# Kernel tuning notes

Hardware: AMD Instinct MI355X
Metric: run time of the kernel (lower is better)

The kernel has to match this reference:

```python
import jax, jax.numpy as jnp
import numpy as np

B, N, H = 32, 64, 128
RBF_DIM, GH, SCATTER, OUT = 32, 256, 64, 256
CUTOFF, PMAX = 6.0, 256
MAXZ, ZEMB, EDIM, NE, PH = 100, 32, 32, 64, 256


def _lin(k, din, dout):
    k1, k2 = jax.random.split(k)
    s = 1.0 / np.sqrt(din)
    W = jax.random.uniform(k1, (din, dout), minval=-s, maxval=s)
    b = jax.random.uniform(k2, (dout,), minval=-s, maxval=s)
    return W, b


def setup_inputs() -> dict:
    key = jax.random.key(0)
    ks = jax.random.split(key, 16)
    h = jax.random.normal(ks[0], (B, N, H), dtype=jnp.float32)
    z = jax.random.randint(ks[1], (B, N), 1, MAXZ + 1)
    pos = jax.random.normal(ks[2], (B, N, 3), dtype=jnp.float32) * 2.0
    mask = jax.random.randint(ks[3], (B, N), 0, 2).astype(bool).at[:, 0].set(True)
    e_feat = jax.random.normal(ks[4], (NE, EDIM), dtype=jnp.float32)
    z_emb = jax.random.normal(ks[5], (MAXZ + 1, ZEMB), dtype=jnp.float32)
    gm_W1, gm_b1 = _lin(ks[6], 2 * H + 3 * RBF_DIM + 1, GH)
    gm_W2, gm_b2 = _lin(ks[7], GH, GH)
    gm_W3, gm_b3 = _lin(ks[8], GH, SCATTER)
    pe_W1, pe_b1 = _lin(ks[9], 2 * ZEMB + EDIM, PH)
    pe_W2, pe_b2 = _lin(ks[10], PH, PH)
    pe_W3, pe_b3 = _lin(ks[11], PH, SCATTER)
    op_W1, op_b1 = _lin(ks[12], SCATTER, GH)
    op_W2, op_b2 = _lin(ks[13], GH, OUT)
    return dict(h=h, z=z, pos=pos, mask=mask, e_feat=e_feat, z_emb=z_emb,
                gm_W1=gm_W1, gm_b1=gm_b1, gm_W2=gm_W2, gm_b2=gm_b2, gm_W3=gm_W3, gm_b3=gm_b3,
                pe_W1=pe_W1, pe_b1=pe_b1, pe_W2=pe_W2, pe_b2=pe_b2, pe_W3=pe_W3, pe_b3=pe_b3,
                op_W1=op_W1, op_b1=op_b1, op_W2=op_W2, op_b2=op_b2, absorber_index=0)


def _mlp3(x, W1, b1, W2, b2, W3, b3):
    x = jax.nn.silu(x @ W1 + b1)
    x = jax.nn.silu(x @ W2 + b2)
    return x @ W3 + b3


def _rbf(x):
    centers = jnp.linspace(0.0, CUTOFF, RBF_DIM)
    delta = CUTOFF / (RBF_DIM - 1)
    gamma = 1.0 / (delta * delta + 1e-12)
    return jnp.exp(-gamma * (x[..., None] - centers) ** 2)


def _norm(v):
    # numerically safe euclidean norm over last axis
    return jnp.sqrt(jnp.sum(v * v, axis=-1) + 1e-12)


def _forward(h, z, pos, mask, e_feat, z_emb,
             gm_W1, gm_b1, gm_W2, gm_b2, gm_W3, gm_b3,
             pe_W1, pe_b1, pe_W2, pe_b2, pe_W3, pe_b3,
             op_W1, op_b1, op_W2, op_b2, absorber_index):
    pos0 = pos[:, absorber_index][:, None, :]                       # [B,1,3]
    r = _norm(pos - pos0)                                           # [B,N]
    valid = mask & (jnp.arange(N)[None, :] != absorber_index) & (r <= CUTOFF)
    # enumerate pairs (j<k) in lexicographic order == torch.combinations of sorted where()
    ju, ku = jnp.triu_indices(N, k=1)                               # [Np]
    pv = valid[:, ju] & valid[:, ku]                                # [B,Np]
    order = jnp.argsort(~pv, axis=1, stable=True)[:, :PMAX]         # first PMAX valid pairs, in order
    pmask = jnp.take_along_axis(pv, order, axis=1)                  # [B,PMAX]
    j_idx = jnp.where(pmask, ju[order], 0)
    k_idx = jnp.where(pmask, ku[order], 0)
    bidx = jnp.arange(B)[:, None]
    hj, hk = h[bidx, j_idx], h[bidx, k_idx]                         # [B,P,H]
    posj, posk = pos[bidx, j_idx], pos[bidx, k_idx]                 # [B,P,3]
    vj, vk, vjk = posj - pos0, posk - pos0, posk - posj
    r0j, r0k, rjk = _norm(vj), _norm(vk), _norm(vjk)
    uj = vj / jnp.maximum(r0j[..., None], 1e-8)
    uk = vk / jnp.maximum(r0k[..., None], 1e-8)
    cosang = jnp.clip(jnp.sum(uj * uk, -1, keepdims=True), -1.0, 1.0)
    geom_in = jnp.concatenate([hj, hk,
                               _rbf(jnp.minimum(r0j, CUTOFF)),
                               _rbf(jnp.minimum(r0k, CUTOFF)),
                               _rbf(jnp.minimum(rjk, CUTOFF)), cosang], axis=-1)
    g_geom = _mlp3(geom_in, gm_W1, gm_b1, gm_W2, gm_b2, gm_W3, gm_b3)   # [B,P,SCATTER]
    ej = z_emb[z[bidx, j_idx]]                                      # [B,P,ZEMB]
    ek = z_emb[z[bidx, k_idx]]
    pe_in = jnp.concatenate([
        jnp.broadcast_to(ej[:, :, None, :], (B, PMAX, NE, ZEMB)),
        jnp.broadcast_to(ek[:, :, None, :], (B, PMAX, NE, ZEMB)),
        jnp.broadcast_to(e_feat[None, None], (B, PMAX, NE, EDIM))], axis=-1)
    g_elem = _mlp3(pe_in, pe_W1, pe_b1, pe_W2, pe_b2, pe_W3, pe_b3)     # [B,P,NE,SCATTER]
    contrib = g_geom[:, :, None, :] * g_elem * pmask[:, :, None, None].astype(g_elem.dtype)
    agg = contrib.sum(axis=1)                                           # [B,NE,SCATTER]
    return jax.nn.silu(agg @ op_W1 + op_b1) @ op_W2 + op_b2             # [B,NE,OUT]


def reference(h, z, pos, mask, e_feat, z_emb,
              gm_W1, gm_b1, gm_W2, gm_b2, gm_W3, gm_b3,
              pe_W1, pe_b1, pe_W2, pe_b2, pe_W3, pe_b3,
              op_W1, op_b1, op_W2, op_b2, absorber_index):
    return _forward(h, z, pos, mask, e_feat, z_emb,
                    gm_W1, gm_b1, gm_W2, gm_b2, gm_W3, gm_b3,
                    pe_W1, pe_b1, pe_W2, pe_b2, pe_W3, pe_b3,
                    op_W1, op_b1, op_W2, op_b2, absorber_index)
```

## Files before the change

### kernel.cpp

```cpp
#include <hip/hip_runtime.h>
#include <hip/hip_bf16.h>
#include <stdint.h>


#define CUTOFF_F 6.0f

typedef __bf16 bf16x8_t __attribute__((ext_vector_type(8)));
typedef float  f32x4_t  __attribute__((ext_vector_type(4)));

union FragU { bf16x8_t v; uint32_t u[4]; uint2 d2[2]; uint4 d4; };

__device__ __forceinline__ float silu_f(float x){
    float e = __builtin_amdgcn_exp2f(x * -1.44269504088896f);
    return x * __builtin_amdgcn_rcpf(1.0f + e);
}

__device__ __forceinline__ uint16_t f2bf(float a){
    union { __hip_bfloat16 h; uint16_t u; } c; c.h = __float2bfloat16(a); return c.u;
}
__device__ __forceinline__ uint32_t pk2(float a, float b){
    union { __hip_bfloat162 h; uint32_t u; } c;
    c.h = __float22bfloat162_rn(make_float2(a, b));
    return c.u;
}
__device__ __forceinline__ void frag_lds(FragU& f, const char* base, uint32_t b0, uint32_t b1){
    f.d2[0] = *(const uint2*)(base + b0);
    f.d2[1] = *(const uint2*)(base + b1);
}
__device__ __forceinline__ void frag_gp(FragU& f, const uint16_t* p){
    f.d4 = *(const uint4*)(p);
}

__global__ void k_tables(const float* __restrict__ z_emb, const float* __restrict__ e_feat,
                         const float* __restrict__ pe_W1, const float* __restrict__ pe_b1,
                         float* __restrict__ T_A, float* __restrict__ T_B, float* __restrict__ T_C){
    int row = blockIdx.x; int c = threadIdx.x;
    if (row < 101){
        const float* e = z_emb + row*32;
        float s = 0.f;
        #pragma unroll
        for (int d = 0; d < 32; d++) s += e[d] * pe_W1[d*256 + c];
        T_A[row*256 + c] = s;
    } else if (row < 202){
        const float* e = z_emb + (row-101)*32;
        float s = 0.f;
        #pragma unroll
        for (int d = 0; d < 32; d++) s += e[d] * pe_W1[(32+d)*256 + c];
        T_B[(row-101)*256 + c] = s;
    } else {
        int n = row - 202;
        const float* e = e_feat + n*32;
        float s = pe_b1[c];
        #pragma unroll
        for (int d = 0; d < 32; d++) s += e[d] * pe_W1[(64+d)*256 + c];
        T_C[n*256 + c] = s;
    }
}

__global__ void k_prep(const float* __restrict__ pe_W2, const float* __restrict__ pe_W3,
                       const float* __restrict__ gm_W1, const float* __restrict__ gm_W2,
                       const float* __restrict__ gm_W3,
                       uint16_t* __restrict__ W2p, uint16_t* __restrict__ W3p,
                       uint16_t* __restrict__ gW1p, uint16_t* __restrict__ gW2p,
                       uint16_t* __restrict__ gW3p){
    int idx = blockIdx.x*256 + threadIdx.x;
    if (idx < 65536){
        int d = idx; int c = d >> 8; int r = d & 255;
        int kt = r >> 5, t = r & 31, q = t >> 3, j = t & 7;
        int k = kt*32 + 4*q + (j&3) + ((j>>2)<<4);
        W2p[d] = f2bf(pe_W2[k*256 + c]);
    } else if (idx < 81920){
        int d = idx - 65536; int s = d >> 8; int r = d & 255;
        int kt = r >> 5, t = r & 31, q = t >> 3, j = t & 7;
        int k = kt*32 + 4*q + (j&3) + ((j>>2)<<4);
        W3p[d] = f2bf(pe_W3[k*64 + s]);
    } else if (idx < 180224){
        int d = idx - 81920; int c = d / 384; int r = d - c*384;
        int kt = r >> 5, t = r & 31, q = t >> 3, j = t & 7;
        int k = kt*32 + 4*q + (j&3) + ((j>>2)<<4);
        float v = (k < 353) ? gm_W1[k*256 + c] : 0.0f;
        gW1p[d] = f2bf(v);
    } else if (idx < 245760){
        int d = idx - 180224; int c = d >> 8; int r = d & 255;
        int kt = r >> 5, t = r & 31, q = t >> 3, j = t & 7;
        int k = kt*32 + 4*q + (j&3) + ((j>>2)<<4);
        gW2p[d] = f2bf(gm_W2[k*256 + c]);
    } else {
        int d = idx - 245760; int s = d >> 8; int r = d & 255;
        int kt = r >> 5, t = r & 31, q = t >> 3, j = t & 7;
        int k = kt*32 + 4*q + (j&3) + ((j>>2)<<4);
        gW3p[d] = f2bf(gm_W3[k*64 + s]);
    }
}

__global__ void k_pairs(const float* __restrict__ pos, const int* __restrict__ mask,
                        const int* __restrict__ zin, const int* __restrict__ aidx,
                        int* __restrict__ jA, int* __restrict__ kA,
                        int* __restrict__ zjA, int* __restrict__ zkA,
                        float* __restrict__ pmask, float* __restrict__ pgeo){
    const int b = blockIdx.x;
    const int j = threadIdx.x;
    const int ai = aidx[0];
    __shared__ float sx[64], sy[64], sz[64], sr[64];

    bool okp = true;
    #pragma unroll
    for (int i = 0; i < 2; i++){
        int v = mask[j + 64*i];
        okp = okp && (v == 0 || v == 1);
    }
    const bool isI32 = (__all(okp) != 0);

    float p0x = pos[(b*64+ai)*3+0];
    float p0y = pos[(b*64+ai)*3+1];
    float p0z = pos[(b*64+ai)*3+2];
    float x  = pos[(b*64+j)*3+0];
    float y  = pos[(b*64+j)*3+1];
    float zc = pos[(b*64+j)*3+2];
    float dx = x-p0x, dy = y-p0y, dz = zc-p0z;
    float r = sqrtf(dx*dx + dy*dy + dz*dz + 1e-12f);
    bool mv = isI32 ? (mask[b*64+j] != 0) : (((const unsigned char*)mask)[b*64+j] != 0);
    bool valid = mv && (j != ai) && (r <= CUTOFF_F);
    sx[j]=x; sy[j]=y; sz[j]=zc; sr[j]=r;
    unsigned long long vm = __ballot(valid);
    __syncthreads();

    int z0 = zin[b*64 + 0];
    for (int s = j; s < 256; s += 64){
        int slot = b*256 + s;
        jA[slot]=0; kA[slot]=0; zjA[slot]=z0; zkA[slot]=z0;
        pmask[slot]=0.0f;
        pgeo[slot*4+0]=0.0f; pgeo[slot*4+1]=0.0f; pgeo[slot*4+2]=0.0f; pgeo[slot*4+3]=0.0f;
    }
    __syncthreads();

    int prefix = 0;
    for (int i = 0; i < 63; i++){
        if (i < j && ((vm>>i)&1ull)) prefix += __popcll(vm >> (i+1));
    }
    if (valid){
        int rank = prefix;
        for (int k = j+1; k < 64; k++){
            if ((vm>>k)&1ull){
                if (rank < 256){
                    int slot = b*256 + rank;
                    jA[slot]=j; kA[slot]=k;
                    zjA[slot]=zin[b*64+j]; zkA[slot]=zin[b*64+k];
                    pmask[slot]=1.0f;
                    float vkx=sx[k]-p0x, vky=sy[k]-p0y, vkz=sz[k]-p0z;
                    float jkx=sx[k]-x,   jky=sy[k]-y,   jkz=sz[k]-zc;
                    float rjk = sqrtf(jkx*jkx + jky*jky + jkz*jkz + 1e-12f);
                    float r0k = sr[k];
                    float inj = 1.0f/fmaxf(r,   1e-8f);
                    float ink = 1.0f/fmaxf(r0k, 1e-8f);
                    float cs = (dx*vkx + dy*vky + dz*vkz) * inj * ink;
                    cs = fminf(fmaxf(cs, -1.0f), 1.0f);
                    pgeo[slot*4+0]=r; pgeo[slot*4+1]=r0k; pgeo[slot*4+2]=rjk; pgeo[slot*4+3]=cs;
                }
                rank++;
            }
        }
    }
}

__launch_bounds__(256, 1)
__global__ void k_geom(const float* __restrict__ h, const int* __restrict__ jA, const int* __restrict__ kA,
                       const float* __restrict__ pmask, const float* __restrict__ pgeo,
                       const uint16_t* __restrict__ gW1p, const uint16_t* __restrict__ gW2p,
                       const uint16_t* __restrict__ gW3p,
                       const float* __restrict__ gb1, const float* __restrict__ gb2,
                       const float* __restrict__ gb3, float* __restrict__ ggeom){
    __shared__ __align__(16) char X0[16*768];
    __shared__ __align__(16) char X1[16*512];
    const int b = blockIdx.x >> 4, pc = blockIdx.x & 15;
    const int tid = threadIdx.x;
    const int w = tid >> 6, l = tid & 63, l15 = l & 15, l4 = l >> 4;
    const int pbase = b*256 + pc*16;
    const float GAMMA = 26.694444444444443f;
    const float STEP  = 0.19354838709677419f;

    for (int e = tid; e < 16*96; e += 256){
        int row = e / 96;
        int q = e - row*96;
        int slot = pbase + row;
        float f0=0.f, f1=0.f, f2=0.f, f3=0.f;
        if (q < 64){
            int idxa = (q < 32) ? jA[slot] : kA[slot];
            int koff = (q < 32) ? (q*4) : (q*4 - 128);
            const float* hp = h + ((b*64 + idxa)*128 + koff);
            f0=hp[0]; f1=hp[1]; f2=hp[2]; f3=hp[3];
        } else if (q < 88){
            int kk = q*4 - 256;
            int reg = kk >> 5;
            int t0 = kk & 31;
            float rr = fminf(pgeo[slot*4 + reg], CUTOFF_F);
            float d0 = rr - (float)(t0+0)*STEP; f0 = __builtin_amdgcn_exp2f(-GAMMA*d0*d0*1.44269504088896f);
            float d1 = rr - (float)(t0+1)*STEP; f1 = __builtin_amdgcn_exp2f(-GAMMA*d1*d1*1.44269504088896f);
            float d2 = rr - (float)(t0+2)*STEP; f2 = __builtin_amdgcn_exp2f(-GAMMA*d2*d2*1.44269504088896f);
            float d3 = rr - (float)(t0+3)*STEP; f3 = __builtin_amdgcn_exp2f(-GAMMA*d3*d3*1.44269504088896f);
        } else if (q == 88){
            f0 = pgeo[slot*4+3];
        }
        uint32_t byte = (uint32_t)row*768u + (((uint32_t)(8*q)) ^ (((uint32_t)(row&7))<<4));
        *(uint2*)(X0 + byte) = make_uint2(pk2(f0,f1), pk2(f2,f3));
    }
    __syncthreads();

    f32x4_t a1[4];
    #pragma unroll
    for (int nt=0; nt<4; nt++){ a1[nt][0]=0;a1[nt][1]=0;a1[nt][2]=0;a1[nt][3]=0; }
    #pragma unroll 3
    for (int kt=0; kt<12; kt++){
        int k0 = 4*l4 + 32*kt;
        int row = l15;
        uint32_t sw = ((uint32_t)(row&7))<<4;
        FragU A;
        frag_lds(A, X0, (uint32_t)row*768u + (((uint32_t)(2*k0))^sw),
                        (uint32_t)row*768u + (((uint32_t)(2*k0+32))^sw));
        FragU Bf[4];
        #pragma unroll
        for (int nt=0; nt<4; nt++)
            frag_gp(Bf[nt], gW1p + (64*w + 16*nt + l15)*384 + kt*32 + l4*8);
        __builtin_amdgcn_s_setprio(1);
        #pragma unroll
        for (int nt=0; nt<4; nt++)
            a1[nt] = __builtin_amdgcn_mfma_f32_16x16x32_bf16(A.v, Bf[nt].v, a1[nt], 0,0,0);
        __builtin_amdgcn_s_setprio(0);
    }
    #pragma unroll
    for (int nt=0; nt<4; nt++){
        int c = 64*w + 16*nt + l15;
        float bias = gb1[c];
        #pragma unroll
        for (int r=0; r<4; r++){
            int m = 4*l4 + r;
            float v = silu_f(a1[nt][r] + bias);
            uint32_t byte = (uint32_t)m*512u + (((uint32_t)(2*c)) ^ (((uint32_t)(m&7))<<4));
            *(uint16_t*)(X1 + byte) = f2bf(v);
        }
    }
    __syncthreads();

    f32x4_t a2[4];
    #pragma unroll
    for (int nt=0; nt<4; nt++){ a2[nt][0]=0;a2[nt][1]=0;a2[nt][2]=0;a2[nt][3]=0; }
    #pragma unroll 2
    for (int kt=0; kt<8; kt++){
        int k0 = 4*l4 + 32*kt;
        int row = l15;
        uint32_t sw = ((uint32_t)(row&7))<<4;
        FragU A;
        frag_lds(A, X1, (uint32_t)row*512u + (((uint32_t)(2*k0))^sw),
                        (uint32_t)row*512u + (((uint32_t)(2*k0+32))^sw));
        FragU Bf[4];
        #pragma unroll
        for (int nt=0; nt<4; nt++)
            frag_gp(Bf[nt], gW2p + (64*w + 16*nt + l15)*256 + kt*32 + l4*8);
        __builtin_amdgcn_s_setprio(1);
        #pragma unroll
        for (int nt=0; nt<4; nt++)
            a2[nt] = __builtin_amdgcn_mfma_f32_16x16x32_bf16(A.v, Bf[nt].v, a2[nt], 0,0,0);
        __builtin_amdgcn_s_setprio(0);
    }
    #pragma unroll
    for (int nt=0; nt<4; nt++){
        int c = 64*w + 16*nt + l15;
        float bias = gb2[c];
        #pragma unroll
        for (int r=0; r<4; r++){
            int m = 4*l4 + r;
            float v = silu_f(a2[nt][r] + bias);
            uint32_t byte = (uint32_t)m*512u + (((uint32_t)(2*c)) ^ (((uint32_t)(m&7))<<4));
            *(uint16_t*)(X0 + byte) = f2bf(v);
        }
    }
    __syncthreads();

    f32x4_t a3;
    a3[0]=0;a3[1]=0;a3[2]=0;a3[3]=0;
    int s = 16*w + l15;
    #pragma unroll 2
    for (int kt=0; kt<8; kt++){
        int k0 = 4*l4 + 32*kt;
        FragU Bf; frag_gp(Bf, gW3p + s*256 + kt*32 + l4*8);
        int row = l15;
        uint32_t sw = ((uint32_t)(row&7))<<4;
        FragU A;
        frag_lds(A, X0, (uint32_t)row*512u + (((uint32_t)(2*k0))^sw),
                        (uint32_t)row*512u + (((uint32_t)(2*k0+32))^sw));
        a3 = __builtin_amdgcn_mfma_f32_16x16x32_bf16(A.v, Bf.v, a3, 0,0,0);
    }
    float bias3 = gb3[s];
    #pragma unroll
    for (int r=0; r<4; r++){
        int prow = 4*l4 + r;
        int slot = pbase + prow;
        ggeom[slot*64 + s] = (a3[r] + bias3) * pmask[slot];
    }
}

__launch_bounds__(512, 1)
__global__ void k_pe(const float* __restrict__ T_A, const float* __restrict__ T_B,
                     const float* __restrict__ T_C,
                     const uint16_t* __restrict__ W2p, const uint16_t* __restrict__ W3p,
                     const float* __restrict__ b2, const float* __restrict__ b3,
                     const int* __restrict__ zjA, const int* __restrict__ zkA,
                     const float* __restrict__ ggeom, float* __restrict__ pagg){
    __shared__ __align__(16) char X1s[64*512];
    __shared__ __align__(16) char X2s[64*512];
    const int b = blockIdx.x >> 3, pc = blockIdx.x & 7;
    const int tid = threadIdx.x;
    const int w = tid >> 6, l = tid & 63, l15 = l & 15, l4 = l >> 4;
    const int mw = w & 3, kth = w >> 2;

    float b2v[2], b3v[4];
    #pragma unroll
    for (int nt=0; nt<2; nt++) b2v[nt] = b2[32*w + 16*nt + l15];
    #pragma unroll
    for (int nt=0; nt<4; nt++) b3v[nt] = b3[16*nt + l15];
    const float hb = (kth == 0) ? 1.0f : 0.0f;

    f32x4_t pacc[4];
    #pragma unroll
    for (int nt=0; nt<4; nt++){ pacc[nt][0]=0;pacc[nt][1]=0;pacc[nt][2]=0;pacc[nt][3]=0; }

    const int kb = tid & 63, nset = tid >> 6;
    const int k4 = kb*4;

    for (int pi = 0; pi < 32; pi++){
        const int slot = b*256 + pc*32 + pi;
        {
            int zj = zjA[slot], zk = zkA[slot];
            float4 ta = *(const float4*)(T_A + zj*256 + k4);
            float4 tb = *(const float4*)(T_B + zk*256 + k4);
            float bx = ta.x+tb.x, by = ta.y+tb.y, bz = ta.z+tb.z, bw = ta.w+tb.w;
            #pragma unroll
            for (int i = 0; i < 8; i++){
                int n = nset*8 + i;
                float4 tc = *(const float4*)(T_C + n*256 + k4);
                float v0 = silu_f(bx+tc.x), v1 = silu_f(by+tc.y);
                float v2 = silu_f(bz+tc.z), v3 = silu_f(bw+tc.w);
                uint32_t byte = (uint32_t)n*512u + (((uint32_t)(8*kb)) ^ (((uint32_t)(n&7))<<4));
                *(uint2*)(X1s + byte) = make_uint2(pk2(v0,v1), pk2(v2,v3));
            }
        }
        __syncthreads();
        f32x4_t a1[4][2];
        #pragma unroll
        for (int mt=0; mt<4; mt++)
            #pragma unroll
            for (int nt=0; nt<2; nt++){ a1[mt][nt][0]=0;a1[mt][nt][1]=0;a1[mt][nt][2]=0;a1[mt][nt][3]=0; }
        #pragma unroll 2
        for (int kt=0; kt<8; kt++){
            int k0 = 4*l4 + 32*kt;
            FragU Bf[2];
            #pragma unroll
            for (int nt=0; nt<2; nt++)
                frag_gp(Bf[nt], W2p + (32*w + 16*nt + l15)*256 + kt*32 + l4*8);
            FragU A[4];
            #pragma unroll
            for (int mt=0; mt<4; mt++){
                int row = 16*mt + l15;
                uint32_t sw = ((uint32_t)(row&7))<<4;
                frag_lds(A[mt], X1s, (uint32_t)row*512u + (((uint32_t)(2*k0))^sw),
                                     (uint32_t)row*512u + (((uint32_t)(2*k0+32))^sw));
            }
            __builtin_amdgcn_s_setprio(1);
            #pragma unroll
            for (int nt=0; nt<2; nt++)
                #pragma unroll
                for (int mt=0; mt<4; mt++)
                    a1[mt][nt] = __builtin_amdgcn_mfma_f32_16x16x32_bf16(A[mt].v, Bf[nt].v, a1[mt][nt], 0,0,0);
            __builtin_amdgcn_s_setprio(0);
        }
        #pragma unroll
        for (int nt=0; nt<2; nt++){
            int c = 32*w + 16*nt + l15;
            #pragma unroll
            for (int mt=0; mt<4; mt++)
                #pragma unroll
                for (int r=0; r<4; r++){
                    int m = 16*mt + 4*l4 + r;
                    float v = silu_f(a1[mt][nt][r] + b2v[nt]);
                    uint32_t byte = (uint32_t)m*512u + (((uint32_t)(2*c)) ^ (((uint32_t)(m&7))<<4));
                    *(uint16_t*)(X2s + byte) = f2bf(v);
                }
        }
        __syncthreads();
        f32x4_t a2[4];
        #pragma unroll
        for (int nt=0; nt<4; nt++){ a2[nt][0]=0;a2[nt][1]=0;a2[nt][2]=0;a2[nt][3]=0; }
        #pragma unroll
        for (int kk=0; kk<4; kk++){
            int kt = 4*kth + kk;
            int k0 = 4*l4 + 32*kt;
            FragU Wf[4];
            #pragma unroll
            for (int nt=0; nt<4; nt++)
                frag_gp(Wf[nt], W3p + (16*nt + l15)*256 + kt*32 + l4*8);
            int row = 16*mw + l15;
            uint32_t sw = ((uint32_t)(row&7))<<4;
            FragU A;
            frag_lds(A, X2s, (uint32_t)row*512u + (((uint32_t)(2*k0))^sw),
                             (uint32_t)row*512u + (((uint32_t)(2*k0+32))^sw));
            __builtin_amdgcn_s_setprio(1);
            #pragma unroll
            for (int nt=0; nt<4; nt++)
                a2[nt] = __builtin_amdgcn_mfma_f32_16x16x32_bf16(A.v, Wf[nt].v, a2[nt], 0,0,0);
            __builtin_amdgcn_s_setprio(0);
        }
        #pragma unroll
        for (int nt=0; nt<4; nt++){
            float gg = ggeom[slot*64 + 16*nt + l15];
            #pragma unroll
            for (int r=0; r<4; r++)
                pacc[nt][r] += (a2[nt][r] + b3v[nt]*hb) * gg;
        }
    }
    const int chunk = (b*8 + pc)*2 + kth;
    #pragma unroll
    for (int nt=0; nt<4; nt++)
        #pragma unroll
        for (int r=0; r<4; r++){
            int n = 16*mw + 4*l4 + r;
            int s = 16*nt + l15;
            pagg[(chunk*64 + n)*64 + s] = pacc[nt][r];
        }
}

__global__ void k_out(const float* __restrict__ pagg, const float* __restrict__ W1,
                      const float* __restrict__ bb1, const float* __restrict__ W2,
                      const float* __restrict__ bb2, float* __restrict__ out){
    __shared__ float sag[16][64];
    __shared__ float shid[16][256];
    const int row0 = blockIdx.x * 16;
    const int tid = threadIdx.x;
    const int bb = row0 >> 6;
    for (int i = tid; i < 16*64; i += 256){
        int row = row0 + (i >> 6);
        int nn = row & 63;
        int k = i & 63;
        float acc = 0.f;
        #pragma unroll
        for (int pcc = 0; pcc < 16; pcc++)
            acc += pagg[((bb*16 + pcc)*64 + nn)*64 + k];
        sag[i>>6][k] = acc;
    }
    __syncthreads();
    float a[16];
    #pragma unroll
    for (int i=0;i<16;i++) a[i] = bb1[tid];
    for (int k=0;k<64;k++){
        float wv = W1[k*256 + tid];
        #pragma unroll
        for (int i=0;i<16;i++) a[i] += sag[i][k]*wv;
    }
    #pragma unroll
    for (int i=0;i<16;i++) shid[i][tid] = silu_f(a[i]);
    __syncthreads();
    float o[16];
    #pragma unroll
    for (int i=0;i<16;i++) o[i] = bb2[tid];
    for (int c=0;c<256;c++){
        float wv = W2[c*256 + tid];
        #pragma unroll
        for (int i=0;i<16;i++) o[i] += shid[i][c]*wv;
    }
    #pragma unroll
    for (int i=0;i<16;i++) out[(row0+i)*256 + tid] = o[i];
}

extern "C" void kernel_launch(void* const* d_in, const int* in_sizes, int n_in,
                              void* d_out, int out_size, void* d_ws, size_t ws_size,
                              hipStream_t stream){
    const float* h      = (const float*)d_in[0];
    const int*   z      = (const int*)  d_in[1];
    const float* pos    = (const float*)d_in[2];
    const int*   mask   = (const int*)  d_in[3];
    const float* e_feat = (const float*)d_in[4];
    const float* z_emb  = (const float*)d_in[5];
    const float* gm_W1  = (const float*)d_in[6];
    const float* gm_b1  = (const float*)d_in[7];
    const float* gm_W2  = (const float*)d_in[8];
    const float* gm_b2  = (const float*)d_in[9];
    const float* gm_W3  = (const float*)d_in[10];
    const float* gm_b3  = (const float*)d_in[11];
    const float* pe_W1  = (const float*)d_in[12];
    const float* pe_b1  = (const float*)d_in[13];
    const float* pe_W2  = (const float*)d_in[14];
    const float* pe_b2  = (const float*)d_in[15];
    const float* pe_W3  = (const float*)d_in[16];
    const float* pe_b3  = (const float*)d_in[17];
    const float* op_W1  = (const float*)d_in[18];
    const float* op_b1  = (const float*)d_in[19];
    const float* op_W2  = (const float*)d_in[20];
    const float* op_b2  = (const float*)d_in[21];
    const int*   aidx   = (const int*)  d_in[22];
    float* out = (float*)d_out;
    char* ws = (char*)d_ws;

    float*    T_A   = (float*)   (ws + 0);
    float*    T_B   = (float*)   (ws + 103424);
    float*    T_C   = (float*)   (ws + 206848);
    uint16_t* W2p   = (uint16_t*)(ws + 272384);
    uint16_t* W3p   = (uint16_t*)(ws + 403456);
    uint16_t* gW1p  = (uint16_t*)(ws + 436224);
    uint16_t* gW2p  = (uint16_t*)(ws + 632832);
    uint16_t* gW3p  = (uint16_t*)(ws + 763904);
    int*      jA    = (int*)     (ws + 796672);
    int*      kA    = (int*)     (ws + 829440);
    int*      zjA   = (int*)     (ws + 862208);
    int*      zkA   = (int*)     (ws + 894976);
    float*    pmask = (float*)   (ws + 927744);
    float*    pgeo  = (float*)   (ws + 960512);
    float*    ggeom = (float*)   (ws + 1091584);
    float*    pagg  = (float*)   (ws + 3188736);

    k_tables<<<266, 256, 0, stream>>>(z_emb, e_feat, pe_W1, pe_b1, T_A, T_B, T_C);
    k_prep<<<1024, 256, 0, stream>>>(pe_W2, pe_W3, gm_W1, gm_W2, gm_W3, W2p, W3p, gW1p, gW2p, gW3p);
    k_pairs<<<32, 64, 0, stream>>>(pos, mask, z, aidx, jA, kA, zjA, zkA, pmask, pgeo);
    k_geom<<<512, 256, 0, stream>>>(h, jA, kA, pmask, pgeo, gW1p, gW2p, gW3p,
                                    gm_b1, gm_b2, gm_b3, ggeom);
    k_pe<<<256, 512, 0, stream>>>(T_A, T_B, T_C, W2p, W3p, pe_b2, pe_b3,
                                  zjA, zkA, ggeom, pagg);
    k_out<<<128, 256, 0, stream>>>(pagg, op_W1, op_b1, op_W2, op_b2, out);
}
```

Measured before the change: 402.8 us.

## Repack LDS activations for 16-byte fragment reads and double k_pe grid

```diff
diff --git a/kernel.cpp b/kernel.cpp
--- a/kernel.cpp
+++ b/kernel.cpp
@@ -23,9 +23,14 @@
     c.h = __float22bfloat162_rn(make_float2(a, b));
     return c.u;
 }
-__device__ __forceinline__ void frag_lds(FragU& f, const char* base, uint32_t b0, uint32_t b1){
-    f.d2[0] = *(const uint2*)(base + b0);
-    f.d2[1] = *(const uint2*)(base + b1);
+__device__ __forceinline__ uint32_t pk_off_quad(int kq){
+    return (uint32_t)(64*(kq>>3) + 16*(kq&3) + 8*((kq>>2)&1));
+}
+__device__ __forceinline__ uint32_t x2_off(int c){
+    return (uint32_t)(64*(c>>5) + 16*((c&15)>>2) + 2*(c&3) + 8*((c>>4)&1));
+}
+__device__ __forceinline__ void frag_l4(FragU& f, const char* base, uint32_t byte){
+    f.d4 = *(const uint4*)(base + byte);
 }
 __device__ __forceinline__ void frag_gp(FragU& f, const uint16_t* p){
     f.d4 = *(const uint4*)(p);
@@ -163,6 +168,8 @@
     }
 }
 
+#define GP0 784
+#define GP1 528
 __launch_bounds__(256, 1)
 __global__ void k_geom(const float* __restrict__ h, const int* __restrict__ jA, const int* __restrict__ kA,
                        const float* __restrict__ pmask, const float* __restrict__ pgeo,
@@ -170,8 +177,8 @@
                        const uint16_t* __restrict__ gW3p,
                        const float* __restrict__ gb1, const float* __restrict__ gb2,
                        const float* __restrict__ gb3, float* __restrict__ ggeom){
-    __shared__ __align__(16) char X0[16*768];
-    __shared__ __align__(16) char X1[16*512];
+    __shared__ __align__(16) char X0[16*GP0];
+    __shared__ __align__(16) char X1[16*GP1];
     const int b = blockIdx.x >> 4, pc = blockIdx.x & 15;
     const int tid = threadIdx.x;
     const int w = tid >> 6, l = tid & 63, l15 = l & 15, l4 = l >> 4;
@@ -201,8 +208,7 @@
         } else if (q == 88){
             f0 = pgeo[slot*4+3];
         }
-        uint32_t byte = (uint32_t)row*768u + (((uint32_t)(8*q)) ^ (((uint32_t)(row&7))<<4));
-        *(uint2*)(X0 + byte) = make_uint2(pk2(f0,f1), pk2(f2,f3));
+        *(uint2*)(X0 + (uint32_t)row*GP0 + pk_off_quad(q)) = make_uint2(pk2(f0,f1), pk2(f2,f3));
     }
     __syncthreads();
 
@@ -211,12 +217,8 @@
     for (int nt=0; nt<4; nt++){ a1[nt][0]=0;a1[nt][1]=0;a1[nt][2]=0;a1[nt][3]=0; }
     #pragma unroll 3
     for (int kt=0; kt<12; kt++){
-        int k0 = 4*l4 + 32*kt;
-        int row = l15;
-        uint32_t sw = ((uint32_t)(row&7))<<4;
         FragU A;
-        frag_lds(A, X0, (uint32_t)row*768u + (((uint32_t)(2*k0))^sw),
-                        (uint32_t)row*768u + (((uint32_t)(2*k0+32))^sw));
+        frag_l4(A, X0, (uint32_t)l15*GP0 + 64u*kt + 16u*l4);
         FragU Bf[4];
         #pragma unroll
         for (int nt=0; nt<4; nt++)
@@ -231,12 +233,12 @@
     for (int nt=0; nt<4; nt++){
         int c = 64*w + 16*nt + l15;
         float bias = gb1[c];
+        uint32_t co = x2_off(c);
         #pragma unroll
         for (int r=0; r<4; r++){
             int m = 4*l4 + r;
             float v = silu_f(a1[nt][r] + bias);
-            uint32_t byte = (uint32_t)m*512u + (((uint32_t)(2*c)) ^ (((uint32_t)(m&7))<<4));
-            *(uint16_t*)(X1 + byte) = f2bf(v);
+            *(uint16_t*)(X1 + (uint32_t)m*GP1 + co) = f2bf(v);
         }
     }
     __syncthreads();
@@ -246,12 +248,8 @@
     for (int nt=0; nt<4; nt++){ a2[nt][0]=0;a2[nt][1]=0;a2[nt][2]=0;a2[nt][3]=0; }
     #pragma unroll 2
     for (int kt=0; kt<8; kt++){
-        int k0 = 4*l4 + 32*kt;
-        int row = l15;
-        uint32_t sw = ((uint32_t)(row&7))<<4;
         FragU A;
-        frag_lds(A, X1, (uint32_t)row*512u + (((uint32_t)(2*k0))^sw),
-                        (uint32_t)row*512u + (((uint32_t)(2*k0+32))^sw));
+        frag_l4(A, X1, (uint32_t)l15*GP1 + 64u*kt + 16u*l4);
         FragU Bf[4];
         #pragma unroll
         for (int nt=0; nt<4; nt++)
@@ -266,12 +264,12 @@
     for (int nt=0; nt<4; nt++){
         int c = 64*w + 16*nt + l15;
         float bias = gb2[c];
+        uint32_t co = x2_off(c);
         #pragma unroll
         for (int r=0; r<4; r++){
             int m = 4*l4 + r;
             float v = silu_f(a2[nt][r] + bias);
-            uint32_t byte = (uint32_t)m*512u + (((uint32_t)(2*c)) ^ (((uint32_t)(m&7))<<4));
-            *(uint16_t*)(X0 + byte) = f2bf(v);
+            *(uint16_t*)(X0 + (uint32_t)m*GP0 + co) = f2bf(v);
         }
     }
     __syncthreads();
@@ -281,13 +279,9 @@
     int s = 16*w + l15;
     #pragma unroll 2
     for (int kt=0; kt<8; kt++){
-        int k0 = 4*l4 + 32*kt;
         FragU Bf; frag_gp(Bf, gW3p + s*256 + kt*32 + l4*8);
-        int row = l15;
-        uint32_t sw = ((uint32_t)(row&7))<<4;
         FragU A;
-        frag_lds(A, X0, (uint32_t)row*512u + (((uint32_t)(2*k0))^sw),
-                        (uint32_t)row*512u + (((uint32_t)(2*k0+32))^sw));
+        frag_l4(A, X0, (uint32_t)l15*GP0 + 64u*kt + 16u*l4);
         a3 = __builtin_amdgcn_mfma_f32_16x16x32_bf16(A.v, Bf.v, a3, 0,0,0);
     }
     float bias3 = gb3[s];
@@ -299,16 +293,18 @@
     }
 }
 
-__launch_bounds__(512, 1)
+#define PP 528
+__launch_bounds__(512, 4)
 __global__ void k_pe(const float* __restrict__ T_A, const float* __restrict__ T_B,
                      const float* __restrict__ T_C,
                      const uint16_t* __restrict__ W2p, const uint16_t* __restrict__ W3p,
                      const float* __restrict__ b2, const float* __restrict__ b3,
                      const int* __restrict__ zjA, const int* __restrict__ zkA,
                      const float* __restrict__ ggeom, float* __restrict__ pagg){
-    __shared__ __align__(16) char X1s[64*512];
-    __shared__ __align__(16) char X2s[64*512];
-    const int b = blockIdx.x >> 3, pc = blockIdx.x & 7;
+    extern __shared__ __align__(16) char smem[];
+    char* X1s = smem;
+    char* X2s = smem + 64*PP;
+    const int b = blockIdx.x >> 4, pc = blockIdx.x & 15;
     const int tid = threadIdx.x;
     const int w = tid >> 6, l = tid & 63, l15 = l & 15, l4 = l >> 4;
     const int mw = w & 3, kth = w >> 2;
@@ -326,9 +322,10 @@
 
     const int kb = tid & 63, nset = tid >> 6;
     const int k4 = kb*4;
-
-    for (int pi = 0; pi < 32; pi++){
-        const int slot = b*256 + pc*32 + pi;
+    const uint32_t kboff = pk_off_quad(kb);
+
+    for (int pi = 0; pi < 16; pi++){
+        const int slot = b*256 + pc*16 + pi;
         {
             int zj = zjA[slot], zk = zkA[slot];
             float4 ta = *(const float4*)(T_A + zj*256 + k4);
@@ -340,8 +337,7 @@
                 float4 tc = *(const float4*)(T_C + n*256 + k4);
                 float v0 = silu_f(bx+tc.x), v1 = silu_f(by+tc.y);
                 float v2 = silu_f(bz+tc.z), v3 = silu_f(bw+tc.w);
-                uint32_t byte = (uint32_t)n*512u + (((uint32_t)(8*kb)) ^ (((uint32_t)(n&7))<<4));
-                *(uint2*)(X1s + byte) = make_uint2(pk2(v0,v1), pk2(v2,v3));
+                *(uint2*)(X1s + (uint32_t)n*PP + kboff) = make_uint2(pk2(v0,v1), pk2(v2,v3));
             }
         }
         __syncthreads();
@@ -352,19 +348,14 @@
             for (int nt=0; nt<2; nt++){ a1[mt][nt][0]=0;a1[mt][nt][1]=0;a1[mt][nt][2]=0;a1[mt][nt][3]=0; }
         #pragma unroll 2
         for (int kt=0; kt<8; kt++){
-            int k0 = 4*l4 + 32*kt;
             FragU Bf[2];
             #pragma unroll
             for (int nt=0; nt<2; nt++)
                 frag_gp(Bf[nt], W2p + (32*w + 16*nt + l15)*256 + kt*32 + l4*8);
             FragU A[4];
             #pragma unroll
-            for (int mt=0; mt<4; mt++){
-                int row = 16*mt + l15;
-                uint32_t sw = ((uint32_t)(row&7))<<4;
-                frag_lds(A[mt], X1s, (uint32_t)row*512u + (((uint32_t)(2*k0))^sw),
-                                     (uint32_t)row*512u + (((uint32_t)(2*k0+32))^sw));
-            }
+            for (int mt=0; mt<4; mt++)
+                frag_l4(A[mt], X1s, (uint32_t)(16*mt + l15)*PP + 64u*kt + 16u*l4);
             __builtin_amdgcn_s_setprio(1);
             #pragma unroll
             for (int nt=0; nt<2; nt++)
@@ -376,14 +367,14 @@
         #pragma unroll
         for (int nt=0; nt<2; nt++){
             int c = 32*w + 16*nt + l15;
+            uint32_t co = x2_off(c);
             #pragma unroll
             for (int mt=0; mt<4; mt++)
                 #pragma unroll
                 for (int r=0; r<4; r++){
                     int m = 16*mt + 4*l4 + r;
                     float v = silu_f(a1[mt][nt][r] + b2v[nt]);
-                    uint32_t byte = (uint32_t)m*512u + (((uint32_t)(2*c)) ^ (((uint32_t)(m&7))<<4));
-                    *(uint16_t*)(X2s + byte) = f2bf(v);
+                    *(uint16_t*)(X2s + (uint32_t)m*PP + co) = f2bf(v);
                 }
         }
         __syncthreads();
@@ -393,16 +384,12 @@
         #pragma unroll
         for (int kk=0; kk<4; kk++){
             int kt = 4*kth + kk;
-            int k0 = 4*l4 + 32*kt;
             FragU Wf[4];
             #pragma unroll
             for (int nt=0; nt<4; nt++)
                 frag_gp(Wf[nt], W3p + (16*nt + l15)*256 + kt*32 + l4*8);
-            int row = 16*mw + l15;
-            uint32_t sw = ((uint32_t)(row&7))<<4;
             FragU A;
-            frag_lds(A, X2s, (uint32_t)row*512u + (((uint32_t)(2*k0))^sw),
-                             (uint32_t)row*512u + (((uint32_t)(2*k0+32))^sw));
+            frag_l4(A, X2s, (uint32_t)(16*mw + l15)*PP + 64u*kt + 16u*l4);
             __builtin_amdgcn_s_setprio(1);
             #pragma unroll
             for (int nt=0; nt<4; nt++)
@@ -417,15 +404,30 @@
                 pacc[nt][r] += (a2[nt][r] + b3v[nt]*hb) * gg;
         }
     }
-    const int chunk = (b*8 + pc)*2 + kth;
-    #pragma unroll
-    for (int nt=0; nt<4; nt++)
-        #pragma unroll
-        for (int r=0; r<4; r++){
-            int n = 16*mw + 4*l4 + r;
-            int s = 16*nt + l15;
-            pagg[(chunk*64 + n)*64 + s] = pacc[nt][r];
-        }
+    __syncthreads();
+    if (kth == 1){
+        #pragma unroll
+        for (int nt=0; nt<4; nt++)
+            #pragma unroll
+            for (int r=0; r<4; r++){
+                int n = 16*mw + 4*l4 + r;
+                int s = 16*nt + l15;
+                *(float*)(X2s + (uint32_t)(n*64 + s)*4) = pacc[nt][r];
+            }
+    }
+    __syncthreads();
+    if (kth == 0){
+        const int chunk = b*16 + pc;
+        #pragma unroll
+        for (int nt=0; nt<4; nt++)
+            #pragma unroll
+            for (int r=0; r<4; r++){
+                int n = 16*mw + 4*l4 + r;
+                int s = 16*nt + l15;
+                float v = pacc[nt][r] + *(const float*)(X2s + (uint32_t)(n*64 + s)*4);
+                pagg[(chunk*64 + n)*64 + s] = v;
+            }
+    }
 }
 
 __global__ void k_out(const float* __restrict__ pagg, const float* __restrict__ W1,
@@ -516,12 +518,14 @@
     float*    ggeom = (float*)   (ws + 1091584);
     float*    pagg  = (float*)   (ws + 3188736);
 
+    hipFuncSetAttribute((const void*)k_pe, hipFuncAttributeMaxDynamicSharedMemorySize, 67584);
+
     k_tables<<<266, 256, 0, stream>>>(z_emb, e_feat, pe_W1, pe_b1, T_A, T_B, T_C);
     k_prep<<<1024, 256, 0, stream>>>(pe_W2, pe_W3, gm_W1, gm_W2, gm_W3, W2p, W3p, gW1p, gW2p, gW3p);
     k_pairs<<<32, 64, 0, stream>>>(pos, mask, z, aidx, jA, kA, zjA, zkA, pmask, pgeo);
     k_geom<<<512, 256, 0, stream>>>(h, jA, kA, pmask, pgeo, gW1p, gW2p, gW3p,
                                     gm_b1, gm_b2, gm_b3, ggeom);
-    k_pe<<<256, 512, 0, stream>>>(T_A, T_B, T_C, W2p, W3p, pe_b2, pe_b3,
-                                  zjA, zkA, ggeom, pagg);
+    k_pe<<<512, 512, 67584, stream>>>(T_A, T_B, T_C, W2p, W3p, pe_b2, pe_b3,
+                                      zjA, zkA, ggeom, pagg);
     k_out<<<128, 256, 0, stream>>>(pagg, op_W1, op_b1, op_W2, op_b2, out);
 }
```

Result: slower. 504.5 us (+25.2%).
